# Kernel optimization log

Hardware: AMD Instinct MI355X
Metric: run time of the kernel (lower is better)

The kernel has to match this reference:

```python
import jax, jax.numpy as jnp
import numpy as np

B, N, D = 8, 4096, 512
NUM_CODES = 8192

def setup_inputs() -> dict:
    key = jax.random.key(0)
    kx, kc = jax.random.split(key)
    x = jax.random.normal(kx, (B, N, D), dtype=jnp.float32)
    codebook = jax.random.normal(kc, (NUM_CODES, D), dtype=jnp.float32)
    return {"x": x, "codebook": codebook}

def reference(x, codebook):
    # x: (B, N, D); codebook: (K, D)
    b = x.shape[0]
    flat = x.reshape(-1, x.shape[-1])  # (B*N, D)
    distances = (
        jnp.sum(flat * flat, axis=1, keepdims=True)
        + jnp.sum(codebook * codebook, axis=1)
        - 2.0 * flat @ codebook.T
    )
    codes = jnp.argmin(distances, axis=1).reshape(b, -1)  # (B, N) int
    return codes
```

## Files before the change

kernel.cpp:

```cpp
#include <hip/hip_runtime.h>
#include <hip/hip_bf16.h>
#include <hip/hip_fp16.h>


#define M_ROWS 32768
#define DDIM   512
#define KCODES 8192
#define NCAND  8

typedef unsigned long long u64;
typedef unsigned int u32;
typedef __attribute__((ext_vector_type(4))) float f32x4;
typedef __attribute__((ext_vector_type(8))) int v8i;

#define GL2LDS(gp, lp) __builtin_amdgcn_global_load_lds(                  \
    (const __attribute__((address_space(1))) void*)(gp),                  \
    (__attribute__((address_space(3))) void*)(lp), 16, 0, 0)

__device__ __forceinline__ u32 umin32(u32 a, u32 b) { return a < b ? a : b; }
__device__ __forceinline__ u32 umax32(u32 a, u32 b) { return a > b ? a : b; }
__device__ __forceinline__ u64 umin64(u64 a, u64 b) { return a < b ? a : b; }
__device__ __forceinline__ u32 umin3(u32 a, u32 b, u32 c) {
  return umin32(umin32(a, b), c);
}
__device__ __forceinline__ u32 med3u(u32 a, u32 b, u32 c) {
  u32 d;
  asm("v_med3_u32 %0, %1, %2, %3" : "=v"(d) : "v"(a), "v"(b), "v"(c));
  return d;
}

__device__ __forceinline__ u32 fsort(float s) {
  u32 fb = __float_as_uint(s);
  return fb ^ (u32)(((int)fb >> 31) | 0x80000000);
}

__device__ __forceinline__ uint2 pk8_fp8(float4 v0, float4 v1) {
  int lo = 0, hi = 0;
  lo = __builtin_amdgcn_cvt_pk_fp8_f32(v0.x, v0.y, lo, false);
  lo = __builtin_amdgcn_cvt_pk_fp8_f32(v0.z, v0.w, lo, true);
  hi = __builtin_amdgcn_cvt_pk_fp8_f32(v1.x, v1.y, hi, false);
  hi = __builtin_amdgcn_cvt_pk_fp8_f32(v1.z, v1.w, hi, true);
  return (uint2){(u32)lo, (u32)hi};
}

__global__ __launch_bounds__(256) void conv_codebook_kernel(
    const float* __restrict__ cb, unsigned char* __restrict__ ch8,
    float* __restrict__ cnh) {
  int wave = (blockIdx.x * 256 + threadIdx.x) >> 6;
  int lane = threadIdx.x & 63;
  if (wave >= KCODES) return;
  const float* src = cb + (size_t)wave * DDIM + lane * 8;
  float4 v0 = *(const float4*)(src);
  float4 v1 = *(const float4*)(src + 4);
  *(uint2*)(ch8 + (size_t)wave * DDIM + lane * 8) = pk8_fp8(v0, v1);
  float ss = v0.x*v0.x + v0.y*v0.y + v0.z*v0.z + v0.w*v0.w
           + v1.x*v1.x + v1.y*v1.y + v1.z*v1.z + v1.w*v1.w;
#pragma unroll
  for (int off = 32; off; off >>= 1) ss += __shfl_xor(ss, off);
  if (lane == 0) cnh[wave] = 0.5f * ss;
}

__global__ __launch_bounds__(256) void conv_x_kernel(
    const float* __restrict__ x, unsigned char* __restrict__ xh8) {
  size_t i = ((size_t)blockIdx.x * 256 + threadIdx.x) * 8;
  float4 v0 = *(const float4*)(x + i);
  float4 v1 = *(const float4*)(x + i + 4);
  *(uint2*)(xh8 + i) = pk8_fp8(v0, v1);
}

__global__ __launch_bounds__(512, 4) void coarse_kernel(
    const unsigned char* __restrict__ xh8, const unsigned char* __restrict__ ch8,
    const float* __restrict__ cnh, uint4* __restrict__ part) {
  __shared__ __align__(16) char smem[33792];
  uint2* tab = (uint2*)(smem + 16384);

  const int tid  = threadIdx.x;
  const int lane = tid & 63;
  const int wid  = tid >> 6;
  const int wm   = wid >> 1, wn = wid & 1;
  const int g    = lane >> 4, l16 = lane & 15;

  const int mblk = blockIdx.x >> 3;
  const int ngrp = blockIdx.x & 7;
  const int row0 = mblk * 128;
  const int colgrp = ngrp * 1024;

  v8i A[2][4];
#pragma unroll
  for (int tm = 0; tm < 2; ++tm) {
    const unsigned char* ap =
        xh8 + (size_t)(row0 + wm * 32 + tm * 16 + l16) * DDIM + g * 32;
#pragma unroll
    for (int c = 0; c < 4; ++c) {
      int4 lo = *(const int4*)(ap + c * 128);
      int4 hi = *(const int4*)(ap + c * 128 + 16);
      A[tm][c][0] = lo.x; A[tm][c][1] = lo.y; A[tm][c][2] = lo.z; A[tm][c][3] = lo.w;
      A[tm][c][4] = hi.x; A[tm][c][5] = hi.y; A[tm][c][6] = hi.z; A[tm][c][7] = hi.w;
    }
  }

  const int scode = tid >> 3;
  const int sgran = (tid & 7) ^ (scode & 7);
  const unsigned char* bsrc =
      ch8 + (size_t)(colgrp + scode) * DDIM + sgran * 16;

  const int brow = wn * 32 + l16;
  const int bsl  = ((g * 2) ^ (l16 & 7)) << 4;
  const int boff = brow * 128 + bsl;

  u32 m1 = ~0u, m2 = ~0u, m3 = ~0u;

  GL2LDS(bsrc, smem + tid * 16);
  __syncthreads();

  for (int nb = 0; nb < 16; ++nb) {
    const int col0 = colgrp + nb * 64;
    u32 codev[2];
    float cn[2];
#pragma unroll
    for (int tn = 0; tn < 2; ++tn) {
      codev[tn] = (u32)(col0 + wn * 32 + tn * 16 + l16);
      cn[tn] = cnh[codev[tn]];
    }

    f32x4 acc[2][2];
#pragma unroll
    for (int tm = 0; tm < 2; ++tm)
#pragma unroll
      for (int tn = 0; tn < 2; ++tn) acc[tm][tn] = (f32x4){0.f, 0.f, 0.f, 0.f};

#pragma unroll
    for (int c = 0; c < 4; ++c) {
      if (c < 3)
        GL2LDS(bsrc + (c + 1) * 128, smem + ((c + 1) & 1) * 8192 + tid * 16);
      else if (nb < 15)
        GL2LDS(bsrc + 32768, smem + tid * 16);

      const char* bL = smem + (c & 1) * 8192;
#pragma unroll
      for (int tn = 0; tn < 2; ++tn) {
        int4 lo = *(const int4*)(bL + boff + tn * 2048);
        int4 hi = *(const int4*)(bL + ((boff + tn * 2048) ^ 16));
        v8i bf;
        bf[0] = lo.x; bf[1] = lo.y; bf[2] = lo.z; bf[3] = lo.w;
        bf[4] = hi.x; bf[5] = hi.y; bf[6] = hi.z; bf[7] = hi.w;
#pragma unroll
        for (int tm = 0; tm < 2; ++tm)
          acc[tm][tn] = __builtin_amdgcn_mfma_scale_f32_16x16x128_f8f6f4(
              A[tm][c], bf, acc[tm][tn],
              0, 0,
              0, 0x7F7F7F7F,
              0, 0x7F7F7F7F);
      }
      __syncthreads();
    }

#pragma unroll
    for (int p = 0; p < 2; ++p) {
      if (wn == p) {
#pragma unroll
        for (int tm = 0; tm < 2; ++tm)
#pragma unroll
          for (int r = 0; r < 4; ++r) {
            float s0 = cn[0] - acc[tm][0][r];
            float s1 = cn[1] - acc[tm][1][r];
            u32 key0 = (__float_as_uint(s0) & 0xFFFFE000u) | codev[0];
            u32 key1 = (__float_as_uint(s1) & 0xFFFFE000u) | codev[1];
            const int row = wm * 32 + tm * 16 + g * 4 + r;
            tab[row * 17 + l16] = (uint2){umin32(key0, key1), umax32(key0, key1)};
          }
      }
      __syncthreads();
      if (tid < 128) {
#pragma unroll
        for (int e = 0; e < 16; ++e) {
          uint2 v = tab[tid * 17 + e];
          u32 a = umax32(m1, v.x);
          m1 = umin32(m1, v.x);
          u32 b = med3u(m2, a, v.y);
          m2 = umin3(m2, a, v.y);
          m3 = umin32(m3, b);
        }
      }
      __syncthreads();
    }

    if ((nb & 3) == 3) {
      if (tid < 128) {
        part[(size_t)(ngrp * 4 + (nb >> 2)) * M_ROWS + row0 + tid] =
            (uint4){m1, m2, m3, 0u};
        m1 = ~0u; m2 = ~0u; m3 = ~0u;
      }
    }
    bsrc += 32768;
  }
}

__global__ __launch_bounds__(256) void merge_kernel(
    const uint4* __restrict__ part, int* __restrict__ cand) {
  const int row = blockIdx.x * 256 + threadIdx.x;
  u32 k[NCAND];
#pragma unroll
  for (int i = 0; i < NCAND; ++i) k[i] = ~0u;
  for (int nb = 0; nb < KCODES / 256; ++nb) {
    uint4 e = part[(size_t)nb * M_ROWS + row];
    u32 t = e.x;
#pragma unroll
    for (int i = 0; i < NCAND; ++i) { u32 mx = umax32(k[i], t); k[i] = umin32(k[i], t); t = mx; }
    t = e.y;
#pragma unroll
    for (int i = 0; i < NCAND; ++i) { u32 mx = umax32(k[i], t); k[i] = umin32(k[i], t); t = mx; }
    t = e.z;
#pragma unroll
    for (int i = 0; i < NCAND; ++i) { u32 mx = umax32(k[i], t); k[i] = umin32(k[i], t); t = mx; }
  }
#pragma unroll
  for (int i = 0; i < NCAND; ++i)
    cand[row * NCAND + i] = (int)(k[i] & 0x1FFFu);
}

__global__ __launch_bounds__(256) void rescore_kernel(
    const float* __restrict__ x, const float* __restrict__ cb,
    const float* __restrict__ cnh, const int* __restrict__ cand,
    int* __restrict__ out) {
  int wave = (blockIdx.x * 256 + threadIdx.x) >> 6;
  int lane = threadIdx.x & 63;
  if (wave >= M_ROWS) return;
  int idx[NCAND];
#pragma unroll
  for (int j = 0; j < NCAND; ++j) idx[j] = cand[wave * NCAND + j];

  const float* xr = x + (size_t)wave * DDIM + lane * 8;
  float4 x0 = *(const float4*)(xr);
  float4 x1 = *(const float4*)(xr + 4);

  float d[NCAND];
#pragma unroll
  for (int j = 0; j < NCAND; ++j) {
    const float* c = cb + (size_t)idx[j] * DDIM + lane * 8;
    float4 a0 = *(const float4*)(c);
    float4 a1 = *(const float4*)(c + 4);
    d[j] = x0.x*a0.x + x0.y*a0.y + x0.z*a0.z + x0.w*a0.w
         + x1.x*a1.x + x1.y*a1.y + x1.z*a1.z + x1.w*a1.w;
  }
#pragma unroll
  for (int off = 32; off; off >>= 1)
#pragma unroll
    for (int j = 0; j < NCAND; ++j) d[j] += __shfl_xor(d[j], off);

  if (lane == 0) {
    u64 best = ~0ull;
#pragma unroll
    for (int j = 0; j < NCAND; ++j) {
      float s = cnh[idx[j]] - d[j];
      u64 key = ((u64)fsort(s) << 32) | (u32)idx[j];
      best = umin64(best, key);
    }
    out[wave] = (int)(u32)best;
  }
}

extern "C" void kernel_launch(void* const* d_in, const int* in_sizes, int n_in,
                              void* d_out, int out_size, void* d_ws, size_t ws_size,
                              hipStream_t stream) {
  const float* x  = (const float*)d_in[0];
  const float* cb = (const float*)d_in[1];
  int* out = (int*)d_out;

  char* ws = (char*)d_ws;
  unsigned char* ch8  = (unsigned char*)(ws);
  unsigned char* xh8  = (unsigned char*)(ws + (size_t)4 * 1024 * 1024);
  float*         cnh  = (float*)(ws + (size_t)20 * 1024 * 1024);
  int*           cand = (int*)(ws + (size_t)20 * 1024 * 1024 + 32 * 1024);
  uint4*         part = (uint4*)(ws + (size_t)22 * 1024 * 1024);

  conv_codebook_kernel<<<KCODES / 4, 256, 0, stream>>>(cb, ch8, cnh);
  conv_x_kernel<<<(M_ROWS * DDIM) / (256 * 8), 256, 0, stream>>>(x, xh8);
  coarse_kernel<<<(M_ROWS / 128) * 8, 512, 0, stream>>>(xh8, ch8, cnh, part);
  merge_kernel<<<M_ROWS / 256, 256, 0, stream>>>(part, cand);
  rescore_kernel<<<M_ROWS / 4, 256, 0, stream>>>(x, cb, cnh, cand, out);
}
```

Measured before the change: 367.7 us.

## Triple-buffer codebook tiles with explicit vmcnt waits and stage norms in LDS

Replaces the double-buffered global-to-LDS prefetch with a three-slot ring. Three chunks are issued up front, and each step waits with `s_waitcnt vmcnt(2)` so two loads stay in flight. `__syncthreads` is replaced by raw `s_barrier` calls fenced with sched_barrier and explicit lgkmcnt waits. The per-group codebook norms are loaded into LDS once instead of read from global memory every block. The intent is to hide load latency behind the MFMAs. The cost is more LDS per block, which may lower occupancy, and prefetches in the final iterations that read past the end of the column group.

```diff
diff --git a/kernel.cpp b/kernel.cpp
--- a/kernel.cpp
+++ b/kernel.cpp
@@ -16,6 +16,11 @@
 #define GL2LDS(gp, lp) __builtin_amdgcn_global_load_lds(                  \
     (const __attribute__((address_space(1))) void*)(gp),                  \
     (__attribute__((address_space(3))) void*)(lp), 16, 0, 0)
+
+#define WAITV2() asm volatile("s_waitcnt vmcnt(2)" ::: "memory")
+#define WAITL()  asm volatile("s_waitcnt lgkmcnt(0)" ::: "memory")
+#define SBAR()   __builtin_amdgcn_sched_barrier(0)
+#define BAR() do { SBAR(); __builtin_amdgcn_s_barrier(); SBAR(); } while (0)
 
 __device__ __forceinline__ u32 umin32(u32 a, u32 b) { return a < b ? a : b; }
 __device__ __forceinline__ u32 umax32(u32 a, u32 b) { return a > b ? a : b; }
@@ -71,8 +76,9 @@
 __global__ __launch_bounds__(512, 4) void coarse_kernel(
     const unsigned char* __restrict__ xh8, const unsigned char* __restrict__ ch8,
     const float* __restrict__ cnh, uint4* __restrict__ part) {
-  __shared__ __align__(16) char smem[33792];
-  uint2* tab = (uint2*)(smem + 16384);
+  __shared__ __align__(16) char smem[46080];
+  float* cnL = (float*)(smem + 24576);
+  uint2* tab = (uint2*)(smem + 28672);
 
   const int tid  = threadIdx.x;
   const int lane = tid & 63;
@@ -99,30 +105,28 @@
     }
   }
 
+  if (tid < 256)
+    *(float4*)(cnL + tid * 4) = *(const float4*)(cnh + colgrp + tid * 4);
+
   const int scode = tid >> 3;
   const int sgran = (tid & 7) ^ (scode & 7);
   const unsigned char* bsrc =
       ch8 + (size_t)(colgrp + scode) * DDIM + sgran * 16;
-
-  const int brow = wn * 32 + l16;
-  const int bsl  = ((g * 2) ^ (l16 & 7)) << 4;
-  const int boff = brow * 128 + bsl;
+  char* ldst = smem + tid * 16;
+
+  const int boff = (wn * 32 + l16) * 128 + (((g * 2) ^ (l16 & 7)) << 4);
 
   u32 m1 = ~0u, m2 = ~0u, m3 = ~0u;
 
-  GL2LDS(bsrc, smem + tid * 16);
-  __syncthreads();
-
+  SBAR();
+  GL2LDS(bsrc +   0, ldst);
+  GL2LDS(bsrc + 128, ldst + 8192);
+  GL2LDS(bsrc + 256, ldst + 16384);
+  SBAR();
+  WAITL();
+
+  int bsel = 0;
   for (int nb = 0; nb < 16; ++nb) {
-    const int col0 = colgrp + nb * 64;
-    u32 codev[2];
-    float cn[2];
-#pragma unroll
-    for (int tn = 0; tn < 2; ++tn) {
-      codev[tn] = (u32)(col0 + wn * 32 + tn * 16 + l16);
-      cn[tn] = cnh[codev[tn]];
-    }
-
     f32x4 acc[2][2];
 #pragma unroll
     for (int tm = 0; tm < 2; ++tm)
@@ -131,12 +135,10 @@
 
 #pragma unroll
     for (int c = 0; c < 4; ++c) {
-      if (c < 3)
-        GL2LDS(bsrc + (c + 1) * 128, smem + ((c + 1) & 1) * 8192 + tid * 16);
-      else if (nb < 15)
-        GL2LDS(bsrc + 32768, smem + tid * 16);
-
-      const char* bL = smem + (c & 1) * 8192;
+      int rb = bsel + c; if (rb >= 3) rb -= 3;
+      WAITV2();
+      BAR();
+      const char* bL = smem + rb * 8192;
 #pragma unroll
       for (int tn = 0; tn < 2; ++tn) {
         int4 lo = *(const int4*)(bL + boff + tn * 2048);
@@ -152,25 +154,37 @@
               0, 0x7F7F7F7F,
               0, 0x7F7F7F7F);
       }
-      __syncthreads();
-    }
-
+      WAITL();
+      BAR();
+      GL2LDS(bsrc + (c == 0 ? 384 : 32768 + (c - 1) * 128), ldst + rb * 8192);
+      SBAR();
+    }
+
+    const int col0 = colgrp + nb * 64;
 #pragma unroll
     for (int p = 0; p < 2; ++p) {
       if (wn == p) {
+        u32 codev[2];
+        float cnv[2];
+#pragma unroll
+        for (int tn = 0; tn < 2; ++tn) {
+          codev[tn] = (u32)(col0 + wn * 32 + tn * 16 + l16);
+          cnv[tn] = cnL[nb * 64 + wn * 32 + tn * 16 + l16];
+        }
 #pragma unroll
         for (int tm = 0; tm < 2; ++tm)
 #pragma unroll
           for (int r = 0; r < 4; ++r) {
-            float s0 = cn[0] - acc[tm][0][r];
-            float s1 = cn[1] - acc[tm][1][r];
+            float s0 = cnv[0] - acc[tm][0][r];
+            float s1 = cnv[1] - acc[tm][1][r];
             u32 key0 = (__float_as_uint(s0) & 0xFFFFE000u) | codev[0];
             u32 key1 = (__float_as_uint(s1) & 0xFFFFE000u) | codev[1];
             const int row = wm * 32 + tm * 16 + g * 4 + r;
             tab[row * 17 + l16] = (uint2){umin32(key0, key1), umax32(key0, key1)};
           }
       }
-      __syncthreads();
+      WAITL();
+      BAR();
       if (tid < 128) {
 #pragma unroll
         for (int e = 0; e < 16; ++e) {
@@ -182,7 +196,7 @@
           m3 = umin32(m3, b);
         }
       }
-      __syncthreads();
+      BAR();
     }
 
     if ((nb & 3) == 3) {
@@ -193,6 +207,7 @@
       }
     }
     bsrc += 32768;
+    bsel = (bsel == 2) ? 0 : bsel + 1;
   }
 }
 
```

Result: no change. 374.6 us (+1.9%).
